# Kernel tuning notes

Hardware: AMD Instinct MI355X
Metric: run time of the kernel (lower is better)

## Reference

```python
import jax, jax.numpy as jnp
import numpy as np

N_NODES = 100000
N_EDGES = 1600000
DIM = 128
N_BUNDLES = 8
BUNDLE_DIM = 4
HIDDEN = 256
TIME = 2


def setup_inputs() -> dict:
    key = jax.random.key(0)
    ks = jax.random.split(key, 8)
    x = jax.random.normal(ks[0], (N_NODES, DIM), dtype=jnp.float32)
    node_rep = jax.random.normal(ks[1], (N_NODES, N_BUNDLES, BUNDLE_DIM, BUNDLE_DIM), dtype=jnp.float32)
    # edge list; ensure every node has out-degree >= 1 so degree norm is finite
    src_extra = jax.random.randint(ks[2], (N_EDGES - N_NODES,), 0, N_NODES)
    src = jnp.concatenate([jnp.arange(N_NODES), src_extra]).astype(jnp.int64)
    dst = jax.random.randint(ks[3], (N_EDGES,), 0, N_NODES).astype(jnp.int64)
    w1 = jax.random.normal(ks[4], (HIDDEN, DIM), dtype=jnp.float32) * (1.0 / np.sqrt(DIM))
    b1 = jnp.zeros((HIDDEN,), dtype=jnp.float32)
    w2 = jax.random.normal(ks[5], (DIM, HIDDEN), dtype=jnp.float32) * (1.0 / np.sqrt(HIDDEN))
    b2 = jnp.zeros((DIM,), dtype=jnp.float32)
    return {"x": x, "node_rep": node_rep, "src": src, "dst": dst,
            "w1": w1, "b1": b1, "w2": w2, "b2": b2}


def reference(x, node_rep, src, dst, w1, b1, w2, b2):
    n = x.shape[0]
    # out-degrees (number of edges with node as source)
    deg = jax.ops.segment_sum(jnp.ones_like(src, dtype=x.dtype), src, num_segments=n)
    # u_mul_v: per-edge product of src and dst degrees -> symmetric norm coefs
    norm_coefs = jax.lax.rsqrt(deg[src] * deg[dst])  # [E]
    # per-bundle rotation: einsum('abcd,abde->abce', node_rep, vf)
    vf = x.reshape(n, N_BUNDLES, BUNDLE_DIM, -1)
    vf = jnp.einsum('nbcd,nbde->nbce', node_rep, vf)
    h = vf.reshape(n, DIM)
    # u_mul_e_sum repeated `time` times: out[dst] += h[src] * coef
    for _ in range(TIME):
        h = jax.ops.segment_sum(h[src] * norm_coefs[:, None], dst, num_segments=n)
    # inverse rotation with transposed node_rep
    vf = h.reshape(n, N_BUNDLES, BUNDLE_DIM, -1)
    vf = jnp.einsum('nbdc,nbde->nbce', node_rep, vf)
    h = vf.reshape(n, DIM)
    # feed-forward (dropout=0, exact GELU as in torch nn.GELU default)
    h = jax.nn.gelu(h @ w1.T + b1, approximate=False)
    return h @ w2.T + b2
```

## Files before the change

kernel.cpp:

```cpp
#include <hip/hip_runtime.h>
#include <hip/hip_bf16.h>
#include <math.h>

#define DIM 128
#define HID 256

typedef short s8x __attribute__((ext_vector_type(8)));
typedef float f4x __attribute__((ext_vector_type(4)));

__device__ __forceinline__ unsigned short f2bf(float f) {
    unsigned int u = __float_as_uint(f);
    u += 0x7FFF + ((u >> 16) & 1);
    return (unsigned short)(u >> 16);
}
__device__ __forceinline__ float bf2f(unsigned short b) {
    return __uint_as_float(((unsigned int)b) << 16);
}
__device__ __forceinline__ float bflo(unsigned int p) {
    return __uint_as_float(p << 16);
}
__device__ __forceinline__ float bfhi(unsigned int p) {
    return __uint_as_float(p & 0xffff0000u);
}


__global__ __launch_bounds__(256) void hist_kernel(
        const int* __restrict__ src, const int* __restrict__ dst,
        int* __restrict__ TD, int* __restrict__ TS, int nE, int nbuck, int chunk) {
    __shared__ int hd[1024], hs[1024];
    const int tid = threadIdx.x, blk = blockIdx.x;
    for (int b = tid; b < nbuck; b += 256) { hd[b] = 0; hs[b] = 0; }
    __syncthreads();
    int beg = blk * chunk, end = min(beg + chunk, nE);
    for (int i = beg + tid; i < end; i += 256) {
        atomicAdd(&hd[dst[i] >> 7], 1);
        atomicAdd(&hs[src[i] >> 7], 1);
    }
    __syncthreads();
    for (int b = tid; b < nbuck; b += 256) {
        TD[b * 256 + blk] = hd[b];
        TS[b * 256 + blk] = hs[b];
    }
}

__global__ void scan_blocks(const int* in, int* out, int* bsums, int n) {
    __shared__ int part[256];
    const int tid = threadIdx.x;
    const int base = blockIdx.x * 1024 + tid * 4;
    int v[4];
    int sum = 0;
#pragma unroll
    for (int k = 0; k < 4; ++k) {
        v[k] = (base + k < n) ? in[base + k] : 0;
        sum += v[k];
    }
    part[tid] = sum;
    __syncthreads();
    for (int off = 1; off < 256; off <<= 1) {
        int t = (tid >= off) ? part[tid - off] : 0;
        __syncthreads();
        part[tid] += t;
        __syncthreads();
    }
    int excl = part[tid] - sum;
    if (tid == 255) bsums[blockIdx.x] = part[255];
#pragma unroll
    for (int k = 0; k < 4; ++k) {
        if (base + k < n) out[base + k] = excl;
        excl += v[k];
    }
}

__global__ void scan_sums(int* bsums, int nb) {
    __shared__ int part[256];
    const int tid = threadIdx.x;
    const int base = tid * 4;
    int v[4];
    int sum = 0;
#pragma unroll
    for (int k = 0; k < 4; ++k) {
        v[k] = (base + k < nb) ? bsums[base + k] : 0;
        sum += v[k];
    }
    part[tid] = sum;
    __syncthreads();
    for (int off = 1; off < 256; off <<= 1) {
        int t = (tid >= off) ? part[tid - off] : 0;
        __syncthreads();
        part[tid] += t;
        __syncthreads();
    }
    int excl = part[tid] - sum;
#pragma unroll
    for (int k = 0; k < 4; ++k) {
        if (base + k < nb) bsums[base + k] = excl;
        excl += v[k];
    }
}

__global__ void scan_add(int* T, const int* __restrict__ bsums, int n2, int half, int E) {
    int i = blockIdx.x * blockDim.x + threadIdx.x;
    if (i < n2) {
        int v = T[i] + bsums[i >> 10];
        T[i] = (i >= half) ? v - E : v;
    }
}

__global__ __launch_bounds__(256) void scatter_edges(
        const int* __restrict__ src, const int* __restrict__ dst,
        const int* __restrict__ TD, const int* __restrict__ TS,
        unsigned long long* __restrict__ pairs, int* __restrict__ srcval,
        int nE, int nbuck, int chunk) {
    __shared__ int cd[1024], cs[1024];
    const int tid = threadIdx.x, blk = blockIdx.x;
    for (int b = tid; b < nbuck; b += 256) {
        cd[b] = TD[b * 256 + blk];
        cs[b] = TS[b * 256 + blk];
    }
    __syncthreads();
    int beg = blk * chunk, end = min(beg + chunk, nE);
    for (int i = beg + tid; i < end; i += 256) {
        int s = src[i], d = dst[i];
        int pd = atomicAdd(&cd[d >> 7], 1);
        pairs[pd] = ((unsigned long long)(unsigned)s << 32) | (unsigned)d;
        int ps = atomicAdd(&cs[s >> 7], 1);
        srcval[ps] = s;
    }
}

__global__ __launch_bounds__(256) void finalize_kernel(
        const unsigned long long* __restrict__ pairs, const int* __restrict__ TD,
        const int* __restrict__ srcval, const int* __restrict__ TS,
        int* __restrict__ rowstart, int* __restrict__ esrc,
        float* __restrict__ rdeg, int nE, int nbuck, int nN) {
    __shared__ int hist[128], sbuf[128], cur[128];
    const int tid = threadIdx.x, b = blockIdx.x;
    int beg = TD[b * 256];
    int end = (b + 1 < nbuck) ? TD[(b + 1) * 256] : nE;
    if (tid < 128) hist[tid] = 0;
    __syncthreads();
    for (int i = beg + tid; i < end; i += 256)
        atomicAdd(&hist[(int)((unsigned)pairs[i] & 127u)], 1);
    __syncthreads();
    int v = (tid < 128) ? hist[tid] : 0;
    if (tid < 128) sbuf[tid] = v;
    __syncthreads();
    for (int off = 1; off < 128; off <<= 1) {
        int t = (tid < 128 && tid >= off) ? sbuf[tid - off] : 0;
        __syncthreads();
        if (tid < 128) sbuf[tid] += t;
        __syncthreads();
    }
    if (tid < 128) {
        int excl = sbuf[tid] - v;
        cur[tid] = excl;
        int idx = (b << 7) + tid;
        if (idx <= nN) rowstart[idx] = beg + excl;
    }
    __syncthreads();
    for (int i = beg + tid; i < end; i += 256) {
        unsigned long long p = pairs[i];
        int l = (int)((unsigned)p & 127u);
        int s = (int)(p >> 32);
        int pos = atomicAdd(&cur[l], 1);
        esrc[beg + pos] = s;
    }
    __syncthreads();
    if (tid < 128) hist[tid] = 0;
    __syncthreads();
    int beg2 = TS[b * 256];
    int end2 = (b + 1 < nbuck) ? TS[(b + 1) * 256] : nE;
    for (int i = beg2 + tid; i < end2; i += 256)
        atomicAdd(&hist[srcval[i] & 127], 1);
    __syncthreads();
    if (tid < 128) {
        int idx = (b << 7) + tid;
        if (idx < nN) rdeg[idx] = rsqrtf((float)hist[tid]);
    }
}

__global__ void rot_cvt_kernel(const float* __restrict__ x, const float* __restrict__ R,
                               unsigned short* __restrict__ h0,
                               const float* __restrict__ w1, const float* __restrict__ w2,
                               unsigned short* __restrict__ w1b, unsigned short* __restrict__ w2b,
                               int n, int nbRot) {
    if ((int)blockIdx.x >= nbRot) {
        int t = (blockIdx.x - nbRot) * 256 + threadIdx.x;
        for (int i = t; i < 32768; i += 4096) {
            w1b[i] = f2bf(w1[i]);
            w2b[i] = f2bf(w2[i]);
        }
        return;
    }
    int u = blockIdx.x * blockDim.x + threadIdx.x;
    if (u >= n * 8) return;
    int nd = u >> 3, b = u & 7;
    const float* xp = &x[(size_t)nd * DIM + b * 16];
    const float* Rp = &R[(size_t)nd * DIM + b * 16];
    float xv[16], rv[16];
#pragma unroll
    for (int d = 0; d < 4; ++d) {
        *(float4*)&xv[d * 4] = *(const float4*)&xp[d * 4];
        *(float4*)&rv[d * 4] = *(const float4*)&Rp[d * 4];
    }
    unsigned short ob[16];
#pragma unroll
    for (int c = 0; c < 4; ++c)
#pragma unroll
        for (int e = 0; e < 4; ++e) {
            float acc = 0.f;
#pragma unroll
            for (int d = 0; d < 4; ++d) acc += rv[c * 4 + d] * xv[d * 4 + e];
            ob[c * 4 + e] = f2bf(acc);
        }
    unsigned short* op = &h0[(size_t)nd * DIM + b * 16];
    *(s8x*)&op[0] = *(s8x*)&ob[0];
    *(s8x*)&op[8] = *(s8x*)&ob[8];
}

__global__ __launch_bounds__(256) void gather_kernel(
        const unsigned short* __restrict__ hsrc, const int* __restrict__ esrc,
        const float* __restrict__ rdeg, const int* __restrict__ rowstart,
        unsigned short* __restrict__ hdst, int n) {
    int node = blockIdx.x * 8 + (threadIdx.x >> 5);
    int lane = threadIdx.x & 31;
    if (node >= n) return;
    int beg = rowstart[node];
    int end = rowstart[node + 1];
    float rd = rdeg[node];
    float a0 = 0.f, a1 = 0.f, a2 = 0.f, a3 = 0.f;
    int i = beg;
    for (; i + 2 <= end; i += 2) {
        int s0 = esrc[i], s1 = esrc[i + 1];
        float c0 = rdeg[s0] * rd;
        float c1 = rdeg[s1] * rd;
        uint2 p0 = *(const uint2*)&hsrc[(size_t)s0 * DIM + lane * 4];
        uint2 p1 = *(const uint2*)&hsrc[(size_t)s1 * DIM + lane * 4];
        a0 += bflo(p0.x) * c0 + bflo(p1.x) * c1;
        a1 += bfhi(p0.x) * c0 + bfhi(p1.x) * c1;
        a2 += bflo(p0.y) * c0 + bflo(p1.y) * c1;
        a3 += bfhi(p0.y) * c0 + bfhi(p1.y) * c1;
    }
    if (i < end) {
        int s0 = esrc[i];
        float c0 = rdeg[s0] * rd;
        uint2 p0 = *(const uint2*)&hsrc[(size_t)s0 * DIM + lane * 4];
        a0 += bflo(p0.x) * c0;
        a1 += bfhi(p0.x) * c0;
        a2 += bflo(p0.y) * c0;
        a3 += bfhi(p0.y) * c0;
    }
    uint2 packed;
    packed.x = (unsigned int)f2bf(a0) | ((unsigned int)f2bf(a1) << 16);
    packed.y = (unsigned int)f2bf(a2) | ((unsigned int)f2bf(a3) << 16);
    *(uint2*)&hdst[(size_t)node * DIM + lane * 4] = packed;
}

#define ABST 136
#define HBST 264
__global__ __launch_bounds__(256, 3) void ffn_kernel(
        const unsigned short* __restrict__ h,
        const float* __restrict__ R,
        const unsigned short* __restrict__ w1b,
        const float* __restrict__ b1,
        const unsigned short* __restrict__ w2b,
        const float* __restrict__ b2,
        float* __restrict__ out, int n) {
    __shared__ unsigned short abuf[64 * ABST];
    __shared__ unsigned short hbuf[64 * HBST];
    const int tid  = threadIdx.x;
    const int node0 = blockIdx.x * 64;
    const int wave = tid >> 6;
    const int lane = tid & 63;
    const int lr = lane & 15;
    const int lq = lane >> 4;

    for (int u = tid; u < 512; u += 256) {
        int nd = u >> 3, b = u & 7;
        int gn = node0 + nd;
        float hv[16], rv[16];
        if (gn < n) {
            const unsigned short* hp = &h[(size_t)gn * DIM + b * 16];
            const float* Rp = &R[(size_t)gn * DIM + b * 16];
            unsigned short hraw[16];
            *(s8x*)&hraw[0] = *(const s8x*)&hp[0];
            *(s8x*)&hraw[8] = *(const s8x*)&hp[8];
#pragma unroll
            for (int d = 0; d < 16; ++d) hv[d] = bf2f(hraw[d]);
#pragma unroll
            for (int d = 0; d < 4; ++d)
                *(float4*)&rv[d * 4] = *(const float4*)&Rp[d * 4];
        } else {
#pragma unroll
            for (int d = 0; d < 16; ++d) { hv[d] = 0.f; rv[d] = 0.f; }
        }
#pragma unroll
        for (int c = 0; c < 4; ++c) {
            unsigned short gb[4];
#pragma unroll
            for (int e = 0; e < 4; ++e) {
                float acc = 0.f;
#pragma unroll
                for (int d = 0; d < 4; ++d) acc += rv[d * 4 + c] * hv[d * 4 + e];
                gb[e] = f2bf(acc);
            }
            *(ushort4*)&abuf[nd * ABST + b * 16 + c * 4] =
                make_ushort4(gb[0], gb[1], gb[2], gb[3]);
        }
    }
    __syncthreads();

    f4x acc1[4][4];
#pragma unroll
    for (int mt = 0; mt < 4; ++mt)
#pragma unroll
        for (int nt = 0; nt < 4; ++nt) acc1[mt][nt] = (f4x){0.f, 0.f, 0.f, 0.f};

    const int nw = wave * 64;
    for (int ks = 0; ks < 4; ++ks) {
        const int k0 = ks * 32 + lq * 8;
        s8x af[4], bf[4];
#pragma unroll
        for (int mt = 0; mt < 4; ++mt)
            af[mt] = *(const s8x*)&abuf[(mt * 16 + lr) * ABST + k0];
#pragma unroll
        for (int nt = 0; nt < 4; ++nt)
            bf[nt] = *(const s8x*)&w1b[(size_t)(nw + nt * 16 + lr) * 128 + k0];
#pragma unroll
        for (int mt = 0; mt < 4; ++mt)
#pragma unroll
            for (int nt = 0; nt < 4; ++nt)
                acc1[mt][nt] = __builtin_amdgcn_mfma_f32_16x16x32_bf16(
                    af[mt], bf[nt], acc1[mt][nt], 0, 0, 0);
    }
#pragma unroll
    for (int nt = 0; nt < 4; ++nt) {
        int nn = nw + nt * 16 + lr;
        float bias = b1[nn];
#pragma unroll
        for (int mt = 0; mt < 4; ++mt) {
#pragma unroll
            for (int r = 0; r < 4; ++r) {
                float v = acc1[mt][nt][r] + bias;
                v = 0.5f * v * (1.f + erff(v * 0.70710678118654752f));
                hbuf[(mt * 16 + lq * 4 + r) * HBST + nn] = f2bf(v);
            }
        }
    }
    __syncthreads();

    f4x acc2[4][2];
#pragma unroll
    for (int mt = 0; mt < 4; ++mt)
#pragma unroll
        for (int nt = 0; nt < 2; ++nt) acc2[mt][nt] = (f4x){0.f, 0.f, 0.f, 0.f};

    const int nw2 = wave * 32;
    for (int ks = 0; ks < 8; ++ks) {
        const int k0 = ks * 32 + lq * 8;
        s8x af[4], bf2v[2];
#pragma unroll
        for (int mt = 0; mt < 4; ++mt)
            af[mt] = *(const s8x*)&hbuf[(mt * 16 + lr) * HBST + k0];
#pragma unroll
        for (int nt = 0; nt < 2; ++nt)
            bf2v[nt] = *(const s8x*)&w2b[(size_t)(nw2 + nt * 16 + lr) * 256 + k0];
#pragma unroll
        for (int mt = 0; mt < 4; ++mt)
#pragma unroll
            for (int nt = 0; nt < 2; ++nt)
                acc2[mt][nt] = __builtin_amdgcn_mfma_f32_16x16x32_bf16(
                    af[mt], bf2v[nt], acc2[mt][nt], 0, 0, 0);
    }
#pragma unroll
    for (int nt = 0; nt < 2; ++nt) {
        int n2 = nw2 + nt * 16 + lr;
        float bias = b2[n2];
#pragma unroll
        for (int mt = 0; mt < 4; ++mt) {
#pragma unroll
            for (int r = 0; r < 4; ++r) {
                int gn = node0 + mt * 16 + lq * 4 + r;
                if (gn < n) out[(size_t)gn * DIM + n2] = acc2[mt][nt][r] + bias;
            }
        }
    }
}

extern "C" void kernel_launch(void* const* d_in, const int* in_sizes, int n_in,
                              void* d_out, int out_size, void* d_ws, size_t ws_size,
                              hipStream_t stream) {
    const float* x   = (const float*)d_in[0];
    const float* R   = (const float*)d_in[1];
    const int*   src = (const int*)d_in[2];
    const int*   dst = (const int*)d_in[3];
    const float* w1  = (const float*)d_in[4];
    const float* b1  = (const float*)d_in[5];
    const float* w2  = (const float*)d_in[6];
    const float* b2  = (const float*)d_in[7];
    float* out = (float*)d_out;

    const int N = in_sizes[0] / DIM;
    const int E = in_sizes[2];

    const int nbuck = (N + 127) >> 7;
    const int chunk = (E + 255) / 256;
    const int nScan = nbuck * 256;
    const int nScan2 = 2 * nScan;
    const int nbScan2 = (nScan2 + 1023) / 1024;

    unsigned short* hA = (unsigned short*)d_ws;
    unsigned short* hM = hA + (size_t)N * DIM;
    unsigned long long* pairs = (unsigned long long*)hM;
    int* srcval = (int*)(pairs + E);
    float* rdeg     = (float*)(hM + (size_t)N * DIM);
    int*   rowstart = (int*)(rdeg + N);
    int*   esrc     = rowstart + (N + 1);
    int*   TD       = esrc + E;
    int*   TS       = TD + nScan;
    int*   bsums    = TS + nScan;
    unsigned short* w1b = (unsigned short*)(bsums + 1024);
    unsigned short* w2b = w1b + 32768;

    const int BLK = 256;

    hist_kernel<<<256, BLK, 0, stream>>>(src, dst, TD, TS, E, nbuck, chunk);
    scan_blocks<<<nbScan2, BLK, 0, stream>>>(TD, TD, bsums, nScan2);
    scan_sums<<<1, BLK, 0, stream>>>(bsums, nbScan2);
    scan_add<<<(nScan2 + BLK - 1) / BLK, BLK, 0, stream>>>(TD, bsums, nScan2, nScan, E);
    scatter_edges<<<256, BLK, 0, stream>>>(src, dst, TD, TS, pairs, srcval, E, nbuck, chunk);
    finalize_kernel<<<nbuck, BLK, 0, stream>>>(pairs, TD, srcval, TS, rowstart, esrc, rdeg, E, nbuck, N);

    const int nbRot = ((size_t)N * 8 + BLK - 1) / BLK;
    rot_cvt_kernel<<<nbRot + 16, BLK, 0, stream>>>(x, R, hA, w1, w2, w1b, w2b, N, nbRot);

    gather_kernel<<<(N + 7) / 8, BLK, 0, stream>>>(hA, esrc, rdeg, rowstart, hM, N);
    gather_kernel<<<(N + 7) / 8, BLK, 0, stream>>>(hM, esrc, rdeg, rowstart, hA, N);

    ffn_kernel<<<(N + 63) / 64, BLK, 0, stream>>>(hA, R, w1b, b1, w2b, b2, out, N);
}
```

Before: 444.0 us.

## Fuse second gather into FFN kernel and compute degrees via global atomics

The second neighbor-aggregation pass now runs inside the FFN kernel, which gathers each block's 64 rows into shared memory. This avoids writing and re-reading the intermediate bf16 feature buffer and drops one kernel launch. Out-degrees are now counted with global atomics instead of a second bucket sort, which halves the scan size. Edge pairs are packed into 32 bits, and the shared buffers in the FFN kernel are aliased so occupancy can rise to 4 blocks per CU. In exchange, the FFN blocks take on latency-bound irregular gathers, and the global atomics on degree counters can contend.

```diff
diff --git a/kernel.cpp b/kernel.cpp
--- a/kernel.cpp
+++ b/kernel.cpp
@@ -24,23 +24,30 @@
 }
 
 
+__global__ void prep_kernel(const float* __restrict__ w1, const float* __restrict__ w2,
+                            unsigned short* __restrict__ w1b, unsigned short* __restrict__ w2b,
+                            int* __restrict__ deg, int nN) {
+    const int t = blockIdx.x * 256 + threadIdx.x;
+    w1b[t] = f2bf(w1[t]);
+    w2b[t] = f2bf(w2[t]);
+    for (int i = t; i < nN; i += 32768) deg[i] = 0;
+}
+
 __global__ __launch_bounds__(256) void hist_kernel(
         const int* __restrict__ src, const int* __restrict__ dst,
-        int* __restrict__ TD, int* __restrict__ TS, int nE, int nbuck, int chunk) {
-    __shared__ int hd[1024], hs[1024];
+        int* __restrict__ TD, int* __restrict__ deg, int nE, int nbuck, int chunk) {
+    __shared__ int hd[1024];
     const int tid = threadIdx.x, blk = blockIdx.x;
-    for (int b = tid; b < nbuck; b += 256) { hd[b] = 0; hs[b] = 0; }
+    for (int b = tid; b < nbuck; b += 256) hd[b] = 0;
     __syncthreads();
     int beg = blk * chunk, end = min(beg + chunk, nE);
     for (int i = beg + tid; i < end; i += 256) {
         atomicAdd(&hd[dst[i] >> 7], 1);
-        atomicAdd(&hs[src[i] >> 7], 1);
-    }
-    __syncthreads();
-    for (int b = tid; b < nbuck; b += 256) {
+        atomicAdd(&deg[src[i]], 1);
+    }
+    __syncthreads();
+    for (int b = tid; b < nbuck; b += 256)
         TD[b * 256 + blk] = hd[b];
-        TS[b * 256 + blk] = hs[b];
-    }
 }
 
 __global__ void scan_blocks(const int* in, int* out, int* bsums, int n) {
@@ -98,41 +105,33 @@
     }
 }
 
-__global__ void scan_add(int* T, const int* __restrict__ bsums, int n2, int half, int E) {
+__global__ void scan_add(int* T, const int* __restrict__ bsums, int n,
+                         const int* __restrict__ deg, float* __restrict__ rdeg, int nN) {
     int i = blockIdx.x * blockDim.x + threadIdx.x;
-    if (i < n2) {
-        int v = T[i] + bsums[i >> 10];
-        T[i] = (i >= half) ? v - E : v;
-    }
+    if (i < n) T[i] += bsums[i >> 10];
+    if (i < nN) rdeg[i] = rsqrtf((float)deg[i]);
 }
 
 __global__ __launch_bounds__(256) void scatter_edges(
         const int* __restrict__ src, const int* __restrict__ dst,
-        const int* __restrict__ TD, const int* __restrict__ TS,
-        unsigned long long* __restrict__ pairs, int* __restrict__ srcval,
+        const int* __restrict__ TD, unsigned int* __restrict__ pairs,
         int nE, int nbuck, int chunk) {
-    __shared__ int cd[1024], cs[1024];
+    __shared__ int cd[1024];
     const int tid = threadIdx.x, blk = blockIdx.x;
-    for (int b = tid; b < nbuck; b += 256) {
-        cd[b] = TD[b * 256 + blk];
-        cs[b] = TS[b * 256 + blk];
-    }
+    for (int b = tid; b < nbuck; b += 256) cd[b] = TD[b * 256 + blk];
     __syncthreads();
     int beg = blk * chunk, end = min(beg + chunk, nE);
     for (int i = beg + tid; i < end; i += 256) {
         int s = src[i], d = dst[i];
         int pd = atomicAdd(&cd[d >> 7], 1);
-        pairs[pd] = ((unsigned long long)(unsigned)s << 32) | (unsigned)d;
-        int ps = atomicAdd(&cs[s >> 7], 1);
-        srcval[ps] = s;
+        pairs[pd] = ((unsigned int)s << 7) | (unsigned int)(d & 127);
     }
 }
 
 __global__ __launch_bounds__(256) void finalize_kernel(
-        const unsigned long long* __restrict__ pairs, const int* __restrict__ TD,
-        const int* __restrict__ srcval, const int* __restrict__ TS,
+        const unsigned int* __restrict__ pairs, const int* __restrict__ TD,
         int* __restrict__ rowstart, int* __restrict__ esrc,
-        float* __restrict__ rdeg, int nE, int nbuck, int nN) {
+        int nE, int nbuck, int nN) {
     __shared__ int hist[128], sbuf[128], cur[128];
     const int tid = threadIdx.x, b = blockIdx.x;
     int beg = TD[b * 256];
@@ -140,7 +139,7 @@
     if (tid < 128) hist[tid] = 0;
     __syncthreads();
     for (int i = beg + tid; i < end; i += 256)
-        atomicAdd(&hist[(int)((unsigned)pairs[i] & 127u)], 1);
+        atomicAdd(&hist[(int)(pairs[i] & 127u)], 1);
     __syncthreads();
     int v = (tid < 128) ? hist[tid] : 0;
     if (tid < 128) sbuf[tid] = v;
@@ -159,39 +158,15 @@
     }
     __syncthreads();
     for (int i = beg + tid; i < end; i += 256) {
-        unsigned long long p = pairs[i];
-        int l = (int)((unsigned)p & 127u);
-        int s = (int)(p >> 32);
+        unsigned int p = pairs[i];
+        int l = (int)(p & 127u);
         int pos = atomicAdd(&cur[l], 1);
-        esrc[beg + pos] = s;
-    }
-    __syncthreads();
-    if (tid < 128) hist[tid] = 0;
-    __syncthreads();
-    int beg2 = TS[b * 256];
-    int end2 = (b + 1 < nbuck) ? TS[(b + 1) * 256] : nE;
-    for (int i = beg2 + tid; i < end2; i += 256)
-        atomicAdd(&hist[srcval[i] & 127], 1);
-    __syncthreads();
-    if (tid < 128) {
-        int idx = (b << 7) + tid;
-        if (idx < nN) rdeg[idx] = rsqrtf((float)hist[tid]);
+        esrc[beg + pos] = (int)(p >> 7);
     }
 }
 
 __global__ void rot_cvt_kernel(const float* __restrict__ x, const float* __restrict__ R,
-                               unsigned short* __restrict__ h0,
-                               const float* __restrict__ w1, const float* __restrict__ w2,
-                               unsigned short* __restrict__ w1b, unsigned short* __restrict__ w2b,
-                               int n, int nbRot) {
-    if ((int)blockIdx.x >= nbRot) {
-        int t = (blockIdx.x - nbRot) * 256 + threadIdx.x;
-        for (int i = t; i < 32768; i += 4096) {
-            w1b[i] = f2bf(w1[i]);
-            w2b[i] = f2bf(w2[i]);
-        }
-        return;
-    }
+                               unsigned short* __restrict__ h0, int n) {
     int u = blockIdx.x * blockDim.x + threadIdx.x;
     if (u >= n * 8) return;
     int nd = u >> 3, b = u & 7;
@@ -258,55 +233,98 @@
 
 #define ABST 136
 #define HBST 264
-__global__ __launch_bounds__(256, 3) void ffn_kernel(
-        const unsigned short* __restrict__ h,
+__global__ __launch_bounds__(256, 4) void ffn_kernel(
+        const unsigned short* __restrict__ hM,
+        const int* __restrict__ esrc, const float* __restrict__ rdeg,
+        const int* __restrict__ rowstart,
         const float* __restrict__ R,
         const unsigned short* __restrict__ w1b,
         const float* __restrict__ b1,
         const unsigned short* __restrict__ w2b,
         const float* __restrict__ b2,
         float* __restrict__ out, int n) {
-    __shared__ unsigned short abuf[64 * ABST];
-    __shared__ unsigned short hbuf[64 * HBST];
+    __shared__ unsigned short smem[64 * HBST];
+    unsigned short* abuf = smem;
+    unsigned short* hbuf = smem;
     const int tid  = threadIdx.x;
     const int node0 = blockIdx.x * 64;
     const int wave = tid >> 6;
-    const int lane = tid & 63;
-    const int lr = lane & 15;
-    const int lq = lane >> 4;
+    const int lane64 = tid & 63;
+    const int lr = lane64 & 15;
+    const int lq = lane64 >> 4;
+
+    {
+        const int lane = tid & 31;
+        const int sub  = tid >> 5;
+        for (int p = 0; p < 8; ++p) {
+            const int nd = p * 8 + sub;
+            const int gn = node0 + nd;
+            float a0 = 0.f, a1 = 0.f, a2 = 0.f, a3 = 0.f;
+            if (gn < n) {
+                const int beg = rowstart[gn], end = rowstart[gn + 1];
+                const float rd = rdeg[gn];
+                int i = beg;
+                for (; i + 4 <= end; i += 4) {
+                    int s0 = esrc[i], s1 = esrc[i + 1], s2 = esrc[i + 2], s3 = esrc[i + 3];
+                    float c0 = rdeg[s0] * rd, c1 = rdeg[s1] * rd;
+                    float c2 = rdeg[s2] * rd, c3 = rdeg[s3] * rd;
+                    uint2 p0 = *(const uint2*)&hM[(size_t)s0 * DIM + lane * 4];
+                    uint2 p1 = *(const uint2*)&hM[(size_t)s1 * DIM + lane * 4];
+                    uint2 p2 = *(const uint2*)&hM[(size_t)s2 * DIM + lane * 4];
+                    uint2 p3 = *(const uint2*)&hM[(size_t)s3 * DIM + lane * 4];
+                    a0 += bflo(p0.x) * c0 + bflo(p1.x) * c1 + bflo(p2.x) * c2 + bflo(p3.x) * c3;
+                    a1 += bfhi(p0.x) * c0 + bfhi(p1.x) * c1 + bfhi(p2.x) * c2 + bfhi(p3.x) * c3;
+                    a2 += bflo(p0.y) * c0 + bflo(p1.y) * c1 + bflo(p2.y) * c2 + bflo(p3.y) * c3;
+                    a3 += bfhi(p0.y) * c0 + bfhi(p1.y) * c1 + bfhi(p2.y) * c2 + bfhi(p3.y) * c3;
+                }
+                for (; i < end; ++i) {
+                    int s0 = esrc[i];
+                    float c0 = rdeg[s0] * rd;
+                    uint2 p0 = *(const uint2*)&hM[(size_t)s0 * DIM + lane * 4];
+                    a0 += bflo(p0.x) * c0;
+                    a1 += bfhi(p0.x) * c0;
+                    a2 += bflo(p0.y) * c0;
+                    a3 += bfhi(p0.y) * c0;
+                }
+            }
+            uint2 packed;
+            packed.x = (unsigned int)f2bf(a0) | ((unsigned int)f2bf(a1) << 16);
+            packed.y = (unsigned int)f2bf(a2) | ((unsigned int)f2bf(a3) << 16);
+            *(uint2*)&abuf[nd * ABST + lane * 4] = packed;
+        }
+    }
+    __syncthreads();
 
     for (int u = tid; u < 512; u += 256) {
-        int nd = u >> 3, b = u & 7;
-        int gn = node0 + nd;
+        const int nd = u >> 3, b = u & 7;
+        const int gn = node0 + nd;
+        unsigned short hraw[16];
+        *(s8x*)&hraw[0] = *(const s8x*)&abuf[nd * ABST + b * 16];
+        *(s8x*)&hraw[8] = *(const s8x*)&abuf[nd * ABST + b * 16 + 8];
         float hv[16], rv[16];
+#pragma unroll
+        for (int d = 0; d < 16; ++d) hv[d] = bf2f(hraw[d]);
         if (gn < n) {
-            const unsigned short* hp = &h[(size_t)gn * DIM + b * 16];
             const float* Rp = &R[(size_t)gn * DIM + b * 16];
-            unsigned short hraw[16];
-            *(s8x*)&hraw[0] = *(const s8x*)&hp[0];
-            *(s8x*)&hraw[8] = *(const s8x*)&hp[8];
-#pragma unroll
-            for (int d = 0; d < 16; ++d) hv[d] = bf2f(hraw[d]);
 #pragma unroll
             for (int d = 0; d < 4; ++d)
                 *(float4*)&rv[d * 4] = *(const float4*)&Rp[d * 4];
         } else {
 #pragma unroll
-            for (int d = 0; d < 16; ++d) { hv[d] = 0.f; rv[d] = 0.f; }
+            for (int d = 0; d < 16; ++d) rv[d] = 0.f;
         }
-#pragma unroll
-        for (int c = 0; c < 4; ++c) {
-            unsigned short gb[4];
+        unsigned short gb[16];
+#pragma unroll
+        for (int c = 0; c < 4; ++c)
 #pragma unroll
             for (int e = 0; e < 4; ++e) {
                 float acc = 0.f;
 #pragma unroll
                 for (int d = 0; d < 4; ++d) acc += rv[d * 4 + c] * hv[d * 4 + e];
-                gb[e] = f2bf(acc);
+                gb[c * 4 + e] = f2bf(acc);
             }
-            *(ushort4*)&abuf[nd * ABST + b * 16 + c * 4] =
-                make_ushort4(gb[0], gb[1], gb[2], gb[3]);
-        }
+        *(s8x*)&abuf[nd * ABST + b * 16] = *(s8x*)&gb[0];
+        *(s8x*)&abuf[nd * ABST + b * 16 + 8] = *(s8x*)&gb[8];
     }
     __syncthreads();
 
@@ -319,20 +337,22 @@
     const int nw = wave * 64;
     for (int ks = 0; ks < 4; ++ks) {
         const int k0 = ks * 32 + lq * 8;
-        s8x af[4], bf[4];
+        s8x af[4], bfv[4];
 #pragma unroll
         for (int mt = 0; mt < 4; ++mt)
             af[mt] = *(const s8x*)&abuf[(mt * 16 + lr) * ABST + k0];
 #pragma unroll
         for (int nt = 0; nt < 4; ++nt)
-            bf[nt] = *(const s8x*)&w1b[(size_t)(nw + nt * 16 + lr) * 128 + k0];
+            bfv[nt] = *(const s8x*)&w1b[(size_t)(nw + nt * 16 + lr) * 128 + k0];
 #pragma unroll
         for (int mt = 0; mt < 4; ++mt)
 #pragma unroll
             for (int nt = 0; nt < 4; ++nt)
                 acc1[mt][nt] = __builtin_amdgcn_mfma_f32_16x16x32_bf16(
-                    af[mt], bf[nt], acc1[mt][nt], 0, 0, 0);
-    }
+                    af[mt], bfv[nt], acc1[mt][nt], 0, 0, 0);
+    }
+    __syncthreads();
+
 #pragma unroll
     for (int nt = 0; nt < 4; ++nt) {
         int nn = nw + nt * 16 + lr;
@@ -406,36 +426,36 @@
     const int nbuck = (N + 127) >> 7;
     const int chunk = (E + 255) / 256;
     const int nScan = nbuck * 256;
-    const int nScan2 = 2 * nScan;
-    const int nbScan2 = (nScan2 + 1023) / 1024;
+    const int nbScan = (nScan + 1023) / 1024;
 
     unsigned short* hA = (unsigned short*)d_ws;
     unsigned short* hM = hA + (size_t)N * DIM;
-    unsigned long long* pairs = (unsigned long long*)hM;
-    int* srcval = (int*)(pairs + E);
+    unsigned int* pairs = (unsigned int*)hM;
     float* rdeg     = (float*)(hM + (size_t)N * DIM);
-    int*   rowstart = (int*)(rdeg + N);
+    int*   deg      = (int*)(rdeg + N);
+    int*   rowstart = deg + N;
     int*   esrc     = rowstart + (N + 1);
     int*   TD       = esrc + E;
-    int*   TS       = TD + nScan;
-    int*   bsums    = TS + nScan;
+    int*   bsums    = TD + nScan;
     unsigned short* w1b = (unsigned short*)(bsums + 1024);
     unsigned short* w2b = w1b + 32768;
 
     const int BLK = 256;
 
-    hist_kernel<<<256, BLK, 0, stream>>>(src, dst, TD, TS, E, nbuck, chunk);
-    scan_blocks<<<nbScan2, BLK, 0, stream>>>(TD, TD, bsums, nScan2);
-    scan_sums<<<1, BLK, 0, stream>>>(bsums, nbScan2);
-    scan_add<<<(nScan2 + BLK - 1) / BLK, BLK, 0, stream>>>(TD, bsums, nScan2, nScan, E);
-    scatter_edges<<<256, BLK, 0, stream>>>(src, dst, TD, TS, pairs, srcval, E, nbuck, chunk);
-    finalize_kernel<<<nbuck, BLK, 0, stream>>>(pairs, TD, srcval, TS, rowstart, esrc, rdeg, E, nbuck, N);
+    prep_kernel<<<128, BLK, 0, stream>>>(w1, w2, w1b, w2b, deg, N);
+
+    hist_kernel<<<256, BLK, 0, stream>>>(src, dst, TD, deg, E, nbuck, chunk);
+    scan_blocks<<<nbScan, BLK, 0, stream>>>(TD, TD, bsums, nScan);
+    scan_sums<<<1, BLK, 0, stream>>>(bsums, nbScan);
+    scan_add<<<(nScan + BLK - 1) / BLK, BLK, 0, stream>>>(TD, bsums, nScan, deg, rdeg, N);
+    scatter_edges<<<256, BLK, 0, stream>>>(src, dst, TD, pairs, E, nbuck, chunk);
+    finalize_kernel<<<nbuck, BLK, 0, stream>>>(pairs, TD, rowstart, esrc, E, nbuck, N);
 
     const int nbRot = ((size_t)N * 8 + BLK - 1) / BLK;
-    rot_cvt_kernel<<<nbRot + 16, BLK, 0, stream>>>(x, R, hA, w1, w2, w1b, w2b, N, nbRot);
+    rot_cvt_kernel<<<nbRot, BLK, 0, stream>>>(x, R, hA, N);
 
     gather_kernel<<<(N + 7) / 8, BLK, 0, stream>>>(hA, esrc, rdeg, rowstart, hM, N);
-    gather_kernel<<<(N + 7) / 8, BLK, 0, stream>>>(hM, esrc, rdeg, rowstart, hA, N);
-
-    ffn_kernel<<<(N + 63) / 64, BLK, 0, stream>>>(hA, R, w1b, b1, w2b, b2, out, N);
-}
+
+    ffn_kernel<<<(N + 63) / 64, BLK, 0, stream>>>(hM, esrc, rdeg, rowstart, R,
+                                                  w1b, b1, w2b, b2, out, N);
+}
```

New measurement: 477.0 us. +7.4%, slower.
